# Kernel optimization log

Hardware: AMD Instinct MI355X
Metric: run time of the kernel (lower is better)

The kernel has to match this reference:

```python
import jax, jax.numpy as jnp
import numpy as np

B, T, C = 16, 512, 8          # batch, seq_len, channels
S, KSZ = 64, 32               # n_shapelets, kernel_size
EPS = 1e-8


def setup_inputs() -> dict:
    key = jax.random.key(0)
    kx, kk = jax.random.split(key)
    x = jax.random.normal(kx, (B, T, C), dtype=jnp.float32)
    # RandomUniform(-0.05, 0.05) initializer for the shapelet kernel
    kernel = jax.random.uniform(kk, (S, KSZ, C), dtype=jnp.float32, minval=-0.05, maxval=0.05)
    return {"x": x, "kernel": kernel}


def reference(x, kernel):
    # per-sample, per-channel z-normalization over time
    x_mean = jnp.mean(x, axis=1, keepdims=True)
    x_std = jnp.std(x, axis=1, keepdims=True) + EPS
    x_norm = (x - x_mean) / x_std                      # (B, T, C)

    t_out = T - KSZ + 1
    idx = jnp.arange(t_out)[:, None] + jnp.arange(KSZ)[None, :]  # (T_out, KSZ)
    patches = x_norm[:, idx, :]                        # (B, T_out, KSZ, C)
    # tf.image.extract_patches on x[..., None] emits layout (B, T_out, C, KSZ);
    # the original then row-major reshapes that to (B, T_out, KSZ, C). Reproduce exactly.
    patches = jnp.transpose(patches, (0, 1, 3, 2))     # (B, T_out, C, KSZ)
    patches = patches.reshape(B, t_out, KSZ, C)        # faithful reinterpreting reshape

    # per-shapelet z-normalization over (kernel_size, channels)
    k_mean = jnp.mean(kernel, axis=(1, 2), keepdims=True)
    k_std = jnp.std(kernel, axis=(1, 2), keepdims=True) + EPS
    kern = (kernel - k_mean) / k_std                   # (S, KSZ, C)

    # broadcast squared distance, summed over channels only (as in the original)
    diff = patches[:, :, None, :, :] - kern[None, None, :, :, :]  # (B, T_out, S, KSZ, C)
    dist = jnp.sum(diff * diff, axis=-1)               # (B, T_out, S, KSZ)
    # min over the shapelet axis (axis=2 in the original code)
    return jnp.min(dist, axis=2)                       # (B, T_out, KSZ)
```

## Files before the change

kernel.cpp:

```cpp
#include <hip/hip_runtime.h>

#define TOUT_ 481
#define EPS_  1e-8f

typedef __attribute__((ext_vector_type(8))) short bf16x8;
typedef __attribute__((ext_vector_type(4))) float f32x4;

__device__ __forceinline__ unsigned short f2bf(float f) {
  union { float f; unsigned u; } a; a.f = f;
  unsigned r = a.u + 0x7fffu + ((a.u >> 16) & 1u);
  return (unsigned short)(r >> 16);
}
__device__ __forceinline__ float bf2f(unsigned short h) {
  union { unsigned u; float f; } a; a.u = ((unsigned)h) << 16;
  return a.f;
}

__global__ __launch_bounds__(256) void lsd_mfma2(
    const float* __restrict__ x, const float* __restrict__ kern,
    float* __restrict__ out) {
  __shared__ alignas(16) unsigned short Bls[2048];
  __shared__ float kkls[256];
  __shared__ unsigned short lxb[544];
  __shared__ unsigned int   lxp[520];
  __shared__ float wsum[512];
  __shared__ float red[64];
  __shared__ float cstat[16];

  int tid  = threadIdx.x;
  int lane = tid & 63;
  int wv   = tid >> 6;
  int b    = blockIdx.x >> 4;
  int c    = (blockIdx.x >> 1) & 7;
  int th   = blockIdx.x & 1;

  int s = tid >> 2, q = tid & 3;
  const float4* kern4 = reinterpret_cast<const float4*>(kern);
  float4 kv[16];
  #pragma unroll
  for (int u = 0; u < 16; ++u) kv[u] = kern4[s * 64 + q * 16 + u];

  const float4* x4 = reinterpret_cast<const float4*>(x) + b * 1024;
  float4 xv[4];
  #pragma unroll
  for (int u = 0; u < 4; ++u) xv[u] = x4[tid + 256 * u];

  int k2 = 4 * c + q;
  float4 kb0 = kern4[s * 64 + k2 * 2];
  float4 kb1 = kern4[s * 64 + k2 * 2 + 1];

  float ksum = 0.f, ksq = 0.f;
  #pragma unroll
  for (int u = 0; u < 16; ++u) {
    ksum += kv[u].x + kv[u].y + kv[u].z + kv[u].w;
    ksq = fmaf(kv[u].x, kv[u].x, ksq); ksq = fmaf(kv[u].y, kv[u].y, ksq);
    ksq = fmaf(kv[u].z, kv[u].z, ksq); ksq = fmaf(kv[u].w, kv[u].w, ksq);
  }
  ksum += __shfl_xor(ksum, 1, 64); ksq += __shfl_xor(ksq, 1, 64);
  ksum += __shfl_xor(ksum, 2, 64); ksq += __shfl_xor(ksq, 2, 64);
  float kmean = ksum * (1.0f / 256.0f);
  float kvar  = fmaxf(ksq * (1.0f / 256.0f) - kmean * kmean, 0.0f);
  float krstd = 1.0f / (sqrtf(kvar) + EPS_);

  {
    float vv[8] = {kb0.x, kb0.y, kb0.z, kb0.w, kb1.x, kb1.y, kb1.z, kb1.w};
    union { unsigned u[4]; bf16x8 v; } bw;
    float kk = 0.f;
    #pragma unroll
    for (int jj = 0; jj < 4; ++jj) {
      float vn0 = (vv[2 * jj]     - kmean) * krstd;
      float vn1 = (vv[2 * jj + 1] - kmean) * krstd;
      unsigned short n0 = f2bf(-2.0f * vn0);
      unsigned short n1 = f2bf(-2.0f * vn1);
      float vq0 = bf2f(f2bf(vn0));
      float vq1 = bf2f(f2bf(vn1));
      kk = fmaf(vq0, vq0, kk);
      kk = fmaf(vq1, vq1, kk);
      bw.u[jj] = (unsigned)n0 | ((unsigned)n1 << 16);
    }
    *reinterpret_cast<bf16x8*>(&Bls[tid * 8]) = bw.v;
    kkls[tid] = kk;
  }

  float4 s4v = {0, 0, 0, 0}, q4v = {0, 0, 0, 0};
  #pragma unroll
  for (int u = 0; u < 4; ++u) {
    s4v.x += xv[u].x; s4v.y += xv[u].y; s4v.z += xv[u].z; s4v.w += xv[u].w;
    q4v.x = fmaf(xv[u].x, xv[u].x, q4v.x); q4v.y = fmaf(xv[u].y, xv[u].y, q4v.y);
    q4v.z = fmaf(xv[u].z, xv[u].z, q4v.z); q4v.w = fmaf(xv[u].w, xv[u].w, q4v.w);
  }
  #pragma unroll
  for (int m = 2; m <= 32; m <<= 1) {
    s4v.x += __shfl_xor(s4v.x, m, 64); s4v.y += __shfl_xor(s4v.y, m, 64);
    s4v.z += __shfl_xor(s4v.z, m, 64); s4v.w += __shfl_xor(s4v.w, m, 64);
    q4v.x += __shfl_xor(q4v.x, m, 64); q4v.y += __shfl_xor(q4v.y, m, 64);
    q4v.z += __shfl_xor(q4v.z, m, 64); q4v.w += __shfl_xor(q4v.w, m, 64);
  }
  if (lane < 2) {
    int base = wv * 16 + lane * 8;
    red[base + 0] = s4v.x; red[base + 1] = s4v.y;
    red[base + 2] = s4v.z; red[base + 3] = s4v.w;
    red[base + 4] = q4v.x; red[base + 5] = q4v.y;
    red[base + 6] = q4v.z; red[base + 7] = q4v.w;
  }
  __syncthreads();
  if (tid < 8) {
    int g = tid >> 2, cp = tid & 3;
    float sm = 0.f, sq = 0.f;
    #pragma unroll
    for (int w = 0; w < 4; ++w) {
      sm += red[w * 16 + g * 8 + cp];
      sq += red[w * 16 + g * 8 + 4 + cp];
    }
    float mean = sm * (1.0f / 512.0f);
    float var  = fmaxf(sq * (1.0f / 512.0f) - mean * mean, 0.0f);
    cstat[tid]     = mean;
    cstat[8 + tid] = 1.0f / (sqrtf(var) + EPS_);
  }
  __syncthreads();

  if ((tid & 1) == (c >> 2)) {
    float cm = cstat[c], cr = cstat[8 + c];
    #pragma unroll
    for (int u = 0; u < 4; ++u) {
      int t = (tid >> 1) + 128 * u;
      float4 f = xv[u];
      float val = (c & 2) ? ((c & 1) ? f.w : f.z) : ((c & 1) ? f.y : f.x);
      lxb[t] = f2bf((val - cm) * cr);
    }
  }
  if (tid < 32) lxb[512 + tid] = 0;
  __syncthreads();

  int l15 = lane & 15, kch = lane >> 4;
  bool match = (kch == (l15 & 3));
  bf16x8 Bf[16];
  f32x4  cin[16];
  #pragma unroll
  for (int g = 0; g < 16; ++g) {
    int so = g * 16 + l15;
    bf16x8 z = {0, 0, 0, 0, 0, 0, 0, 0};
    Bf[g] = match ? *reinterpret_cast<const bf16x8*>(&Bls[so * 8]) : z;
    float kkv = kkls[so];
    cin[g][0] = kkv; cin[g][1] = kkv; cin[g][2] = kkv; cin[g][3] = kkv;
  }

  for (int i = tid; i < 520; i += 256)
    lxp[i] = (unsigned)lxb[i] | ((unsigned)lxb[i + 1] << 16);
  for (int m = tid; m < 512; m += 256) {
    float acc = 0.f;
    #pragma unroll
    for (int j = 0; j < 8; ++j) { float v = bf2f(lxb[m + j]); acc = fmaf(v, v, acc); }
    wsum[m] = acc;
  }
  __syncthreads();

  int NT = th ? 15 : 16;
  int la = l15 + 8 * kch;
  for (int gt = wv; gt < NT; gt += 4) {
    int t0 = th * 248 + gt * 16;
    int p  = t0 + la;
    union { unsigned ui[4]; bf16x8 v; } au;
    au.ui[0] = lxp[p];     au.ui[1] = lxp[p + 2];
    au.ui[2] = lxp[p + 4]; au.ui[3] = lxp[p + 6];

    f32x4 mn = {3.0e38f, 3.0e38f, 3.0e38f, 3.0e38f};
    #pragma unroll
    for (int g = 0; g < 16; ++g) {
      f32x4 d = __builtin_amdgcn_mfma_f32_16x16x32_bf16(au.v, Bf[g], cin[g], 0, 0, 0);
      mn[0] = fminf(mn[0], d[0]); mn[1] = fminf(mn[1], d[1]);
      mn[2] = fminf(mn[2], d[2]); mn[3] = fminf(mn[3], d[3]);
    }
    #pragma unroll
    for (int r = 0; r < 4; ++r) {
      mn[r] = fminf(mn[r], __shfl_xor(mn[r], 4, 64));
      mn[r] = fminf(mn[r], __shfl_xor(mn[r], 8, 64));
    }
    int o = lane & 3;
    float ma = (lane & 4) ? mn[1] : mn[0];
    float mb = (lane & 4) ? mn[3] : mn[2];
    float mv = (lane & 8) ? mb : ma;
    int t = t0 + (lane >> 4) * 4 + ((lane >> 2) & 3);
    if (t < TOUT_)
      out[(b * TOUT_ + t) * 32 + c * 4 + o] = wsum[t + 8 * o] + mv;
  }
}

extern "C" void kernel_launch(void* const* d_in, const int* in_sizes, int n_in,
                              void* d_out, int out_size, void* d_ws, size_t ws_size,
                              hipStream_t stream) {
  const float* x    = (const float*)d_in[0];
  const float* kern = (const float*)d_in[1];
  float* out = (float*)d_out;
  lsd_mfma2<<<256, 256, 0, stream>>>(x, kern, out);
}
```

Measured before the change: 13.40 us.

## Merge time-half blocks into one 512-thread block per batch-channel

Removes the split of each (batch, channel) pair across two blocks. One 512-thread block now covers all output tiles, so the per-block kernel normalization and x statistics are computed once instead of twice. Each thread loads half as many kernel and x values, and only the threads owning the current channel's shapelet slice write B fragments. The cost is half as many blocks (128 on a GPU with many CUs), which lowers parallelism, and the 16x16 tiles are spread over 8 waves, most of which get 3 or 4 tiles.

```diff
diff --git a/kernel.cpp b/kernel.cpp
--- a/kernel.cpp
+++ b/kernel.cpp
@@ -16,78 +16,85 @@
   return a.f;
 }
 
-__global__ __launch_bounds__(256) void lsd_mfma2(
+__global__ __launch_bounds__(512) void lsd_mfma3(
     const float* __restrict__ x, const float* __restrict__ kern,
     float* __restrict__ out) {
   __shared__ alignas(16) unsigned short Bls[2048];
   __shared__ float kkls[256];
   __shared__ unsigned short lxb[544];
-  __shared__ unsigned int   lxp[520];
+  __shared__ unsigned int   lxp[528];
   __shared__ float wsum[512];
-  __shared__ float red[64];
+  __shared__ float red[128];
   __shared__ float cstat[16];
 
   int tid  = threadIdx.x;
   int lane = tid & 63;
   int wv   = tid >> 6;
-  int b    = blockIdx.x >> 4;
-  int c    = (blockIdx.x >> 1) & 7;
-  int th   = blockIdx.x & 1;
-
-  int s = tid >> 2, q = tid & 3;
+  int b    = blockIdx.x >> 3;
+  int c    = blockIdx.x & 7;
+
+  int s = tid >> 3, q8 = tid & 7;
   const float4* kern4 = reinterpret_cast<const float4*>(kern);
-  float4 kv[16];
-  #pragma unroll
-  for (int u = 0; u < 16; ++u) kv[u] = kern4[s * 64 + q * 16 + u];
-
+  float4 kvA[8];
+  #pragma unroll
+  for (int m = 0; m < 4; ++m) {
+    int j = q8 + 8 * m;
+    kvA[2 * m]     = kern4[s * 64 + 2 * j];
+    kvA[2 * m + 1] = kern4[s * 64 + 2 * j + 1];
+  }
   const float4* x4 = reinterpret_cast<const float4*>(x) + b * 1024;
-  float4 xv[4];
-  #pragma unroll
-  for (int u = 0; u < 4; ++u) xv[u] = x4[tid + 256 * u];
-
-  int k2 = 4 * c + q;
-  float4 kb0 = kern4[s * 64 + k2 * 2];
-  float4 kb1 = kern4[s * 64 + k2 * 2 + 1];
+  float4 xv0 = x4[tid];
+  float4 xv1 = x4[tid + 512];
 
   float ksum = 0.f, ksq = 0.f;
   #pragma unroll
-  for (int u = 0; u < 16; ++u) {
-    ksum += kv[u].x + kv[u].y + kv[u].z + kv[u].w;
-    ksq = fmaf(kv[u].x, kv[u].x, ksq); ksq = fmaf(kv[u].y, kv[u].y, ksq);
-    ksq = fmaf(kv[u].z, kv[u].z, ksq); ksq = fmaf(kv[u].w, kv[u].w, ksq);
+  for (int u = 0; u < 8; ++u) {
+    float4 f = kvA[u];
+    ksum += f.x + f.y + f.z + f.w;
+    ksq = fmaf(f.x, f.x, ksq); ksq = fmaf(f.y, f.y, ksq);
+    ksq = fmaf(f.z, f.z, ksq); ksq = fmaf(f.w, f.w, ksq);
   }
   ksum += __shfl_xor(ksum, 1, 64); ksq += __shfl_xor(ksq, 1, 64);
   ksum += __shfl_xor(ksum, 2, 64); ksq += __shfl_xor(ksq, 2, 64);
+  ksum += __shfl_xor(ksum, 4, 64); ksq += __shfl_xor(ksq, 4, 64);
   float kmean = ksum * (1.0f / 256.0f);
   float kvar  = fmaxf(ksq * (1.0f / 256.0f) - kmean * kmean, 0.0f);
   float krstd = 1.0f / (sqrtf(kvar) + EPS_);
 
   {
-    float vv[8] = {kb0.x, kb0.y, kb0.z, kb0.w, kb1.x, kb1.y, kb1.z, kb1.w};
-    union { unsigned u[4]; bf16x8 v; } bw;
-    float kk = 0.f;
-    #pragma unroll
-    for (int jj = 0; jj < 4; ++jj) {
-      float vn0 = (vv[2 * jj]     - kmean) * krstd;
-      float vn1 = (vv[2 * jj + 1] - kmean) * krstd;
-      unsigned short n0 = f2bf(-2.0f * vn0);
-      unsigned short n1 = f2bf(-2.0f * vn1);
-      float vq0 = bf2f(f2bf(vn0));
-      float vq1 = bf2f(f2bf(vn1));
-      kk = fmaf(vq0, vq0, kk);
-      kk = fmaf(vq1, vq1, kk);
-      bw.u[jj] = (unsigned)n0 | ((unsigned)n1 << 16);
-    }
-    *reinterpret_cast<bf16x8*>(&Bls[tid * 8]) = bw.v;
-    kkls[tid] = kk;
+    int o_own = (q8 - 4 * c) & 7;
+    if (o_own < 4) {
+      int m_own = (4 * c + o_own - q8) >> 3;
+      float4 pa = kvA[2 * m_own], pb = kvA[2 * m_own + 1];
+      float vv[8] = {pa.x, pa.y, pa.z, pa.w, pb.x, pb.y, pb.z, pb.w};
+      union { unsigned u[4]; bf16x8 v; } bw;
+      float kk = 0.f;
+      #pragma unroll
+      for (int jj = 0; jj < 4; ++jj) {
+        float vn0 = (vv[2 * jj]     - kmean) * krstd;
+        float vn1 = (vv[2 * jj + 1] - kmean) * krstd;
+        unsigned short n0 = f2bf(-2.0f * vn0);
+        unsigned short n1 = f2bf(-2.0f * vn1);
+        float vq0 = bf2f(f2bf(vn0));
+        float vq1 = bf2f(f2bf(vn1));
+        kk = fmaf(vq0, vq0, kk);
+        kk = fmaf(vq1, vq1, kk);
+        bw.u[jj] = (unsigned)n0 | ((unsigned)n1 << 16);
+      }
+      int so = s * 4 + o_own;
+      *reinterpret_cast<bf16x8*>(&Bls[so * 8]) = bw.v;
+      kkls[so] = kk;
+    }
   }
 
   float4 s4v = {0, 0, 0, 0}, q4v = {0, 0, 0, 0};
-  #pragma unroll
-  for (int u = 0; u < 4; ++u) {
-    s4v.x += xv[u].x; s4v.y += xv[u].y; s4v.z += xv[u].z; s4v.w += xv[u].w;
-    q4v.x = fmaf(xv[u].x, xv[u].x, q4v.x); q4v.y = fmaf(xv[u].y, xv[u].y, q4v.y);
-    q4v.z = fmaf(xv[u].z, xv[u].z, q4v.z); q4v.w = fmaf(xv[u].w, xv[u].w, q4v.w);
+  {
+    s4v.x = xv0.x + xv1.x; s4v.y = xv0.y + xv1.y;
+    s4v.z = xv0.z + xv1.z; s4v.w = xv0.w + xv1.w;
+    q4v.x = fmaf(xv0.x, xv0.x, xv1.x * xv1.x);
+    q4v.y = fmaf(xv0.y, xv0.y, xv1.y * xv1.y);
+    q4v.z = fmaf(xv0.z, xv0.z, xv1.z * xv1.z);
+    q4v.w = fmaf(xv0.w, xv0.w, xv1.w * xv1.w);
   }
   #pragma unroll
   for (int m = 2; m <= 32; m <<= 1) {
@@ -108,7 +115,7 @@
     int g = tid >> 2, cp = tid & 3;
     float sm = 0.f, sq = 0.f;
     #pragma unroll
-    for (int w = 0; w < 4; ++w) {
+    for (int w = 0; w < 8; ++w) {
       sm += red[w * 16 + g * 8 + cp];
       sq += red[w * 16 + g * 8 + 4 + cp];
     }
@@ -121,13 +128,11 @@
 
   if ((tid & 1) == (c >> 2)) {
     float cm = cstat[c], cr = cstat[8 + c];
-    #pragma unroll
-    for (int u = 0; u < 4; ++u) {
-      int t = (tid >> 1) + 128 * u;
-      float4 f = xv[u];
-      float val = (c & 2) ? ((c & 1) ? f.w : f.z) : ((c & 1) ? f.y : f.x);
-      lxb[t] = f2bf((val - cm) * cr);
-    }
+    int t = tid >> 1;
+    float v0 = (c & 2) ? ((c & 1) ? xv0.w : xv0.z) : ((c & 1) ? xv0.y : xv0.x);
+    float v1 = (c & 2) ? ((c & 1) ? xv1.w : xv1.z) : ((c & 1) ? xv1.y : xv1.x);
+    lxb[t]       = f2bf((v0 - cm) * cr);
+    lxb[t + 256] = f2bf((v1 - cm) * cr);
   }
   if (tid < 32) lxb[512 + tid] = 0;
   __syncthreads();
@@ -145,9 +150,10 @@
     cin[g][0] = kkv; cin[g][1] = kkv; cin[g][2] = kkv; cin[g][3] = kkv;
   }
 
-  for (int i = tid; i < 520; i += 256)
+  for (int i = tid; i < 528; i += 512)
     lxp[i] = (unsigned)lxb[i] | ((unsigned)lxb[i + 1] << 16);
-  for (int m = tid; m < 512; m += 256) {
+  {
+    int m = tid;
     float acc = 0.f;
     #pragma unroll
     for (int j = 0; j < 8; ++j) { float v = bf2f(lxb[m + j]); acc = fmaf(v, v, acc); }
@@ -155,10 +161,9 @@
   }
   __syncthreads();
 
-  int NT = th ? 15 : 16;
   int la = l15 + 8 * kch;
-  for (int gt = wv; gt < NT; gt += 4) {
-    int t0 = th * 248 + gt * 16;
+  for (int gt = wv; gt < 31; gt += 8) {
+    int t0 = gt * 16;
     int p  = t0 + la;
     union { unsigned ui[4]; bf16x8 v; } au;
     au.ui[0] = lxp[p];     au.ui[1] = lxp[p + 2];
@@ -192,5 +197,5 @@
   const float* x    = (const float*)d_in[0];
   const float* kern = (const float*)d_in[1];
   float* out = (float*)d_out;
-  lsd_mfma2<<<256, 256, 0, stream>>>(x, kern, out);
-}
+  lsd_mfma3<<<128, 512, 0, stream>>>(x, kern, out);
+}
```

After: 14.45 us. 1.08x slower.
